# Kernel optimization log

Measured on AMD Instinct MI355X. Metric: run time of the kernel, lower is better.

Reference implementation:

```python
import jax, jax.numpy as jnp
import numpy as np

N_NODES = 100000
N_EDGES = 3200000
F_IN, F_HID, N_ACT = 128, 16, 32


def setup_inputs() -> dict:
    key = jax.random.key(0)
    k1, k2, k3, k4, k5, k6 = jax.random.split(key, 6)
    return {
        "x": jax.random.normal(k1, (N_NODES, F_IN), dtype=jnp.float32),
        "W1": jax.random.normal(k2, (F_IN, F_HID), dtype=jnp.float32) * 0.1,
        "b1": jax.random.normal(k3, (F_HID,), dtype=jnp.float32) * 0.1,
        "W2": jax.random.normal(k4, (F_HID, N_ACT), dtype=jnp.float32) * 0.1,
        "b2": jax.random.normal(k5, (N_ACT,), dtype=jnp.float32) * 0.1,
        "edge_index": jax.random.randint(k6, (2, N_EDGES), 0, N_NODES, dtype=jnp.int64),
    }


def _gcn_layer(h, W, b, src, dst, norm, n):
    # PyG GCNConv: linear first, then normalized scatter-add aggregation, then bias
    h = h @ W                                   # [N, out]
    msg = h[src] * norm[:, None]                # gather + edge scale, [E+N, out]
    agg = jax.ops.segment_sum(msg, dst, num_segments=n)
    return agg + b


def reference(x, W1, b1, W2, b2, edge_index):
    n = x.shape[0]
    loops = jnp.arange(n, dtype=edge_index.dtype)
    src = jnp.concatenate([edge_index[0], loops])  # add self-loops (GCNConv default)
    dst = jnp.concatenate([edge_index[1], loops])
    # symmetric normalization: deg on A + I, norm_e = d_src^-1/2 * d_dst^-1/2
    deg = jax.ops.segment_sum(jnp.ones_like(dst, dtype=x.dtype), dst, num_segments=n)
    dis = jnp.where(deg > 0, jax.lax.rsqrt(deg), 0.0)
    norm = dis[src] * dis[dst]
    h = jax.nn.relu(_gcn_layer(x, W1, b1, src, dst, norm, n))
    return _gcn_layer(h, W2, b2, src, dst, norm, n)
```

## Files before the change

### kernel.cpp

```cpp
#include <hip/hip_runtime.h>
#include <hip/hip_fp16.h>


#define NNODES 100000
#define FIN    128
#define FHID   16
#define NACT   32
#define BUCK   196
#define NB     511
#define MAGIC  21913099u
#define TILE   4096
#define ASTRIDE 17
#define SCALE    262144.0f
#define INVSCALE 3.814697265625e-06f

__device__ __forceinline__ int bucket_of(int d) {
    return (int)__umulhi((unsigned)d, MAGIC);
}

__device__ __forceinline__ unsigned pack2(float a, float b) {
    __half2 h = __floats2half2_rn(a, b);
    return *reinterpret_cast<unsigned*>(&h);
}

__device__ __forceinline__ float2 h2f(unsigned u) {
    return __half22float2(*reinterpret_cast<__half2*>(&u));
}

__device__ __forceinline__ int wave_iscan(int v, int lane) {
#pragma unroll
    for (int d = 1; d < 64; d <<= 1) {
        int u = __shfl_up(v, d, 64);
        if (lane >= d) v += u;
    }
    return v;
}

__global__ void k_coarse(const int* __restrict__ dst, int E, int* __restrict__ bcnt,
                         unsigned short* __restrict__ thist) {
    __shared__ int hist[NB];
    int t = threadIdx.x;
    int tb = blockIdx.x * TILE;
    int tn = min(TILE, E - tb);
    for (int i = t; i < NB; i += 256) hist[i] = 0;
    __syncthreads();
    if ((E & 3) == 0) {
        const int4* d4 = (const int4*)(dst + tb);
        int tn4 = tn >> 2;
        for (int i = t; i < tn4; i += 256) {
            int4 v = d4[i];
            atomicAdd(&hist[bucket_of(v.x)], 1);
            atomicAdd(&hist[bucket_of(v.y)], 1);
            atomicAdd(&hist[bucket_of(v.z)], 1);
            atomicAdd(&hist[bucket_of(v.w)], 1);
        }
        for (int i = (tn4 << 2) + t; i < tn; i += 256)
            atomicAdd(&hist[bucket_of(dst[tb + i])], 1);
    } else {
        for (int i = t; i < tn; i += 256)
            atomicAdd(&hist[bucket_of(dst[tb + i])], 1);
    }
    __syncthreads();
    size_t row = (size_t)blockIdx.x * NB;
    for (int i = t; i < NB; i += 256) {
        int hv = hist[i];
        thist[row + i] = (unsigned short)hv;
        if (hv) atomicAdd(&bcnt[i], hv);
    }
}

__global__ void __launch_bounds__(512) k_bin(
        const int* __restrict__ src, const int* __restrict__ dst, int E,
        const int* __restrict__ bcnt, int* __restrict__ gcur,
        const unsigned short* __restrict__ thist,
        int* __restrict__ bptr, unsigned* __restrict__ binned) {
    __shared__ unsigned staged[TILE];
    __shared__ int gscat[TILE];
    __shared__ int lcur[NB];
    __shared__ int dbase[NB];
    __shared__ int bptrS[NB];
    __shared__ int wsum[8];
    int t = threadIdx.x, lane = t & 63, wv = t >> 6;

    int c0 = (t < NB) ? bcnt[t] : 0;
    int incl0 = wave_iscan(c0, lane);
    if (lane == 63) wsum[wv] = incl0;
    __syncthreads();
    int add0 = 0;
#pragma unroll
    for (int i = 0; i < 8; ++i) add0 += (i < wv) ? wsum[i] : 0;
    incl0 += add0;
    int excl0 = incl0 - c0;
    if (t < NB) bptrS[t] = excl0;
    if (blockIdx.x == 0) {
        if (t < NB) bptr[t] = excl0;
        if (t == NB) bptr[NB] = excl0;
    }
    __syncthreads();

    int tb = blockIdx.x * TILE;
    int tn = min(TILE, E - tb);
    size_t row = (size_t)blockIdx.x * NB;
    int c = (t < NB) ? (int)thist[row + t] : 0;
    int incl = wave_iscan(c, lane);
    if (lane == 63) wsum[wv] = incl;
    __syncthreads();
    int add = 0;
#pragma unroll
    for (int i = 0; i < 8; ++i) add += (i < wv) ? wsum[i] : 0;
    incl += add;
    int excl = incl - c;
    if (t < NB) {
        lcur[t] = excl;
        int gb = (c > 0) ? atomicAdd(&gcur[t], c) : 0;
        dbase[t] = bptrS[t] + gb - excl;
    }
    __syncthreads();

    if ((E & 3) == 0) {
        const int4* d4 = (const int4*)(dst + tb);
        const int4* s4 = (const int4*)(src + tb);
        int tn4 = tn >> 2;
        for (int i = t; i < tn4; i += 512) {
            int4 dv = d4[i], sv = s4[i];
#pragma unroll
            for (int j = 0; j < 4; ++j) {
                int d = (j == 0) ? dv.x : (j == 1) ? dv.y : (j == 2) ? dv.z : dv.w;
                int s = (j == 0) ? sv.x : (j == 1) ? sv.y : (j == 2) ? sv.z : sv.w;
                int b = bucket_of(d);
                int pos = atomicAdd(&lcur[b], 1);
                staged[pos] = ((unsigned)s << 8) | (unsigned)(d - b * BUCK);
                gscat[pos] = dbase[b] + pos;
            }
        }
        for (int i = (tn4 << 2) + t; i < tn; i += 512) {
            int d = dst[tb + i], s = src[tb + i];
            int b = bucket_of(d);
            int pos = atomicAdd(&lcur[b], 1);
            staged[pos] = ((unsigned)s << 8) | (unsigned)(d - b * BUCK);
            gscat[pos] = dbase[b] + pos;
        }
    } else {
        for (int i = t; i < tn; i += 512) {
            int d = dst[tb + i], s = src[tb + i];
            int b = bucket_of(d);
            int pos = atomicAdd(&lcur[b], 1);
            staged[pos] = ((unsigned)s << 8) | (unsigned)(d - b * BUCK);
            gscat[pos] = dbase[b] + pos;
        }
    }
    __syncthreads();
    for (int j = t; j < tn; j += 512) binned[gscat[j]] = staged[j];
}

#define FMA4(A, S, W) { (A).x += (S) * (W).x; (A).y += (S) * (W).y; \
                        (A).z += (S) * (W).z; (A).w += (S) * (W).w; }

__global__ void __launch_bounds__(256) k_deg_xw1(
        const int* __restrict__ bptr, const unsigned* __restrict__ binned,
        const float* __restrict__ x, const float* __restrict__ W1,
        float* __restrict__ dis, __half* __restrict__ featp, int n) {
    __shared__ int cnt[BUCK];
    __shared__ float sdis[BUCK];
    int t = threadIdx.x;
    int bk = blockIdx.x;
    if (t < BUCK) cnt[t] = 0;
    __syncthreads();
    int beg = bptr[bk], end = bptr[bk + 1];
    for (int i = beg + t; i < end; i += 256) atomicAdd(&cnt[binned[i] & 255], 1);
    __syncthreads();
    int node = bk * BUCK + t;
    if (t < BUCK) {
        float dv = rsqrtf((float)cnt[t] + 1.0f);
        sdis[t] = dv;
        if (node < n) dis[node] = dv;
    }
    __syncthreads();
    if (t >= BUCK || node >= n) return;

    const float4* xr = (const float4*)(x + (size_t)node * FIN);
    const float4* w4 = (const float4*)W1;
    float4 a0 = make_float4(0.f, 0.f, 0.f, 0.f), a1 = a0, a2 = a0, a3 = a0;
#pragma unroll 8
    for (int k4 = 0; k4 < FIN / 4; ++k4) {
        float4 xv = xr[k4];
        int kb = k4 * 16;
        FMA4(a0, xv.x, w4[kb + 0]);  FMA4(a1, xv.x, w4[kb + 1]);
        FMA4(a2, xv.x, w4[kb + 2]);  FMA4(a3, xv.x, w4[kb + 3]);
        FMA4(a0, xv.y, w4[kb + 4]);  FMA4(a1, xv.y, w4[kb + 5]);
        FMA4(a2, xv.y, w4[kb + 6]);  FMA4(a3, xv.y, w4[kb + 7]);
        FMA4(a0, xv.z, w4[kb + 8]);  FMA4(a1, xv.z, w4[kb + 9]);
        FMA4(a2, xv.z, w4[kb + 10]); FMA4(a3, xv.z, w4[kb + 11]);
        FMA4(a0, xv.w, w4[kb + 12]); FMA4(a1, xv.w, w4[kb + 13]);
        FMA4(a2, xv.w, w4[kb + 14]); FMA4(a3, xv.w, w4[kb + 15]);
    }
    float d = sdis[t];
    uint4 w0, w1;
    w0.x = pack2(a0.x * d, a0.y * d); w0.y = pack2(a0.z * d, a0.w * d);
    w0.z = pack2(a1.x * d, a1.y * d); w0.w = pack2(a1.z * d, a1.w * d);
    w1.x = pack2(a2.x * d, a2.y * d); w1.y = pack2(a2.z * d, a2.w * d);
    w1.z = pack2(a3.x * d, a3.y * d); w1.w = pack2(a3.z * d, a3.w * d);
    uint4* hr = (uint4*)(featp + (size_t)node * FHID);
    hr[0] = w0; hr[1] = w1;
}

#define ADD8(U, dptr) { \
    float2 f0_ = h2f((U).x), f1_ = h2f((U).y), f2_ = h2f((U).z), f3_ = h2f((U).w); \
    atomicAdd(&(dptr)[0], __float2int_rn(f0_.x * SCALE)); \
    atomicAdd(&(dptr)[1], __float2int_rn(f0_.y * SCALE)); \
    atomicAdd(&(dptr)[2], __float2int_rn(f1_.x * SCALE)); \
    atomicAdd(&(dptr)[3], __float2int_rn(f1_.y * SCALE)); \
    atomicAdd(&(dptr)[4], __float2int_rn(f2_.x * SCALE)); \
    atomicAdd(&(dptr)[5], __float2int_rn(f2_.y * SCALE)); \
    atomicAdd(&(dptr)[6], __float2int_rn(f3_.x * SCALE)); \
    atomicAdd(&(dptr)[7], __float2int_rn(f3_.y * SCALE)); }

template <int L>
__global__ void __launch_bounds__(512) k_agg(
        const int* __restrict__ bptr, const unsigned* __restrict__ binned,
        const float* __restrict__ dis, const __half* __restrict__ featp,
        const float* __restrict__ W2, const float* __restrict__ bias,
        void* __restrict__ outp, int n) {
    __shared__ int acc[BUCK * ASTRIDE];
    __shared__ float wb[FHID * NACT];
    __shared__ float bs[NACT];
    int t = threadIdx.x;
    int bk = blockIdx.x;
    int base = bk * BUCK;
    int nn = min(BUCK, n - base);
    const uint4* fp4 = (const uint4*)featp;
    if (L == 2) {
        for (int i = t; i < FHID * NACT; i += 512) wb[i] = W2[i];
        if (t < NACT) bs[t] = bias[t];
    }
    for (int idx = t; idx < BUCK * 2; idx += 512) {
        int d = idx >> 1, p2 = idx & 1;
        int* a = &acc[d * ASTRIDE + p2 * 8];
        if (d < nn) {
            uint4 u = fp4[(size_t)((base + d) << 1) + p2];
            float2 f0 = h2f(u.x), f1 = h2f(u.y), f2 = h2f(u.z), f3 = h2f(u.w);
            a[0] = __float2int_rn(f0.x * SCALE);
            a[1] = __float2int_rn(f0.y * SCALE);
            a[2] = __float2int_rn(f1.x * SCALE);
            a[3] = __float2int_rn(f1.y * SCALE);
            a[4] = __float2int_rn(f2.x * SCALE);
            a[5] = __float2int_rn(f2.y * SCALE);
            a[6] = __float2int_rn(f3.x * SCALE);
            a[7] = __float2int_rn(f3.y * SCALE);
        } else {
            a[0] = 0; a[1] = 0; a[2] = 0; a[3] = 0;
            a[4] = 0; a[5] = 0; a[6] = 0; a[7] = 0;
        }
    }
    __syncthreads();
    int beg = bptr[bk], end = bptr[bk + 1];
    int pr = t >> 1, p2 = t & 1;
    int i = beg + pr;
    for (; i + 256 < end; i += 512) {
        unsigned e0 = binned[i];
        unsigned e1 = binned[i + 256];
        uint4 u0 = fp4[(size_t)((e0 >> 8) << 1) + p2];
        uint4 u1 = fp4[(size_t)((e1 >> 8) << 1) + p2];
        int* d0 = &acc[(int)(e0 & 255) * ASTRIDE + p2 * 8];
        ADD8(u0, d0);
        int* d1 = &acc[(int)(e1 & 255) * ASTRIDE + p2 * 8];
        ADD8(u1, d1);
    }
    if (i < end) {
        unsigned e0 = binned[i];
        uint4 u0 = fp4[(size_t)((e0 >> 8) << 1) + p2];
        int* d0 = &acc[(int)(e0 & 255) * ASTRIDE + p2 * 8];
        ADD8(u0, d0);
    }
    __syncthreads();
    if (L == 1) {
        for (int idx = t; idx < nn * 4; idx += 512) {
            int d = idx >> 2, pp = idx & 3;
            int node = base + d;
            float di = dis[node];
            const int* a = &acc[d * ASTRIDE + pp * 4];
            float4 bv = ((const float4*)bias)[pp];
            float f0 = (float)a[0] * INVSCALE;
            float f1 = (float)a[1] * INVSCALE;
            float f2 = (float)a[2] * INVSCALE;
            float f3 = (float)a[3] * INVSCALE;
            float rx = fmaxf(di * f0 + bv.x, 0.f) * di;
            float ry = fmaxf(di * f1 + bv.y, 0.f) * di;
            float rz = fmaxf(di * f2 + bv.z, 0.f) * di;
            float rw = fmaxf(di * f3 + bv.w, 0.f) * di;
            uint2 w;
            w.x = pack2(rx, ry);
            w.y = pack2(rz, rw);
            ((uint2*)outp)[(size_t)node * 4 + pp] = w;
        }
    } else {
        for (int idx = t; idx < nn * 2; idx += 512) {
            int d = idx >> 1, h = idx & 1;
            int node = base + d;
            float di = dis[node];
            float p16[FHID];
#pragma unroll
            for (int c = 0; c < FHID; ++c)
                p16[c] = di * ((float)acc[d * ASTRIDE + c] * INVSCALE);
            float o[16];
#pragma unroll
            for (int j = 0; j < 16; ++j) {
                int col = h * 16 + j;
                float s = bs[col];
#pragma unroll
                for (int c = 0; c < FHID; ++c) s += p16[c] * wb[c * NACT + col];
                o[j] = s;
            }
            float4* orow = (float4*)outp + (size_t)node * 8 + h * 4;
            orow[0] = make_float4(o[0], o[1], o[2], o[3]);
            orow[1] = make_float4(o[4], o[5], o[6], o[7]);
            orow[2] = make_float4(o[8], o[9], o[10], o[11]);
            orow[3] = make_float4(o[12], o[13], o[14], o[15]);
        }
    }
}

extern "C" void kernel_launch(void* const* d_in, const int* in_sizes, int n_in,
                              void* d_out, int out_size, void* d_ws, size_t ws_size,
                              hipStream_t stream) {
    const float* x  = (const float*)d_in[0];
    const float* W1 = (const float*)d_in[1];
    const float* b1 = (const float*)d_in[2];
    const float* W2 = (const float*)d_in[3];
    const float* b2 = (const float*)d_in[4];
    const int*   ei = (const int*)d_in[5];
    const int E = in_sizes[5] / 2;
    const int n = NNODES;
    const int npad = n + 8;
    const int* src = ei;
    const int* dst = ei + E;
    const int ntiles = (E + TILE - 1) / TILE;

    float* fb    = (float*)d_ws;
    float* dis   = fb;
    __half* featp = (__half*)(fb + (size_t)n);
    __half* h1p   = featp + (size_t)16 * npad;
    int*   ib    = (int*)(h1p + (size_t)16 * npad);
    int*   bcnt  = ib;
    int*   gcur  = ib + NB;
    int*   bptr  = ib + 2 * NB;
    size_t thist_off = (size_t)(3 * NB + 1);
    unsigned short* thist = (unsigned short*)(ib + thist_off);
    size_t thist_ints = ((size_t)ntiles * NB + 1) / 2;
    unsigned* binned = (unsigned*)(ib + thist_off + thist_ints);

    (void)hipMemsetAsync(bcnt, 0, 2 * NB * sizeof(int), stream);

    const int B = 256;
    k_coarse<<<ntiles, B, 0, stream>>>(dst, E, bcnt, thist);
    k_bin<<<ntiles, 512, 0, stream>>>(src, dst, E, bcnt, gcur, thist, bptr, binned);
    k_deg_xw1<<<NB, B, 0, stream>>>(bptr, binned, x, W1, dis, featp, n);
    k_agg<1><<<NB, 512, 0, stream>>>(bptr, binned, dis, featp, nullptr, b1, (void*)h1p, n);
    k_agg<2><<<NB, 512, 0, stream>>>(bptr, binned, dis, h1p, W2, b2, d_out, n);
}
```

Before: 214.9 us.

## Compute degrees via global atomics in coarse pass and double binning tile size

Per-node in-degrees are now counted with global atomics in the coarse histogram kernel, so the x@W1 kernel no longer rescans the binned edge list per bucket and can use a flat one-node-per-thread grid. The binning kernel now processes 8192-edge tiles with 1024 threads, merging two coarse tile histograms per block. This trades 3.2M scattered global atomics for removing a full pass over binned edges, and doubles shared memory per bin block, which may reduce occupancy.

```diff
diff --git a/kernel.cpp b/kernel.cpp
--- a/kernel.cpp
+++ b/kernel.cpp
@@ -10,6 +10,7 @@
 #define NB     511
 #define MAGIC  21913099u
 #define TILE   4096
+#define TILE2  8192
 #define ASTRIDE 17
 #define SCALE    262144.0f
 #define INVSCALE 3.814697265625e-06f
@@ -37,7 +38,7 @@
 }
 
 __global__ void k_coarse(const int* __restrict__ dst, int E, int* __restrict__ bcnt,
-                         unsigned short* __restrict__ thist) {
+                         int* __restrict__ deg, unsigned short* __restrict__ thist) {
     __shared__ int hist[NB];
     int t = threadIdx.x;
     int tb = blockIdx.x * TILE;
@@ -49,16 +50,20 @@
         int tn4 = tn >> 2;
         for (int i = t; i < tn4; i += 256) {
             int4 v = d4[i];
-            atomicAdd(&hist[bucket_of(v.x)], 1);
-            atomicAdd(&hist[bucket_of(v.y)], 1);
-            atomicAdd(&hist[bucket_of(v.z)], 1);
-            atomicAdd(&hist[bucket_of(v.w)], 1);
-        }
-        for (int i = (tn4 << 2) + t; i < tn; i += 256)
-            atomicAdd(&hist[bucket_of(dst[tb + i])], 1);
+            atomicAdd(&hist[bucket_of(v.x)], 1); atomicAdd(&deg[v.x], 1);
+            atomicAdd(&hist[bucket_of(v.y)], 1); atomicAdd(&deg[v.y], 1);
+            atomicAdd(&hist[bucket_of(v.z)], 1); atomicAdd(&deg[v.z], 1);
+            atomicAdd(&hist[bucket_of(v.w)], 1); atomicAdd(&deg[v.w], 1);
+        }
+        for (int i = (tn4 << 2) + t; i < tn; i += 256) {
+            int d = dst[tb + i];
+            atomicAdd(&hist[bucket_of(d)], 1); atomicAdd(&deg[d], 1);
+        }
     } else {
-        for (int i = t; i < tn; i += 256)
-            atomicAdd(&hist[bucket_of(dst[tb + i])], 1);
+        for (int i = t; i < tn; i += 256) {
+            int d = dst[tb + i];
+            atomicAdd(&hist[bucket_of(d)], 1); atomicAdd(&deg[d], 1);
+        }
     }
     __syncthreads();
     size_t row = (size_t)blockIdx.x * NB;
@@ -69,17 +74,17 @@
     }
 }
 
-__global__ void __launch_bounds__(512) k_bin(
+__global__ void __launch_bounds__(1024) k_bin(
         const int* __restrict__ src, const int* __restrict__ dst, int E,
         const int* __restrict__ bcnt, int* __restrict__ gcur,
         const unsigned short* __restrict__ thist,
         int* __restrict__ bptr, unsigned* __restrict__ binned) {
-    __shared__ unsigned staged[TILE];
-    __shared__ int gscat[TILE];
+    __shared__ unsigned staged[TILE2];
+    __shared__ int gscat[TILE2];
     __shared__ int lcur[NB];
     __shared__ int dbase[NB];
     __shared__ int bptrS[NB];
-    __shared__ int wsum[8];
+    __shared__ int wsum[16];
     int t = threadIdx.x, lane = t & 63, wv = t >> 6;
 
     int c0 = (t < NB) ? bcnt[t] : 0;
@@ -88,7 +93,7 @@
     __syncthreads();
     int add0 = 0;
 #pragma unroll
-    for (int i = 0; i < 8; ++i) add0 += (i < wv) ? wsum[i] : 0;
+    for (int i = 0; i < 16; ++i) add0 += (i < wv) ? wsum[i] : 0;
     incl0 += add0;
     int excl0 = incl0 - c0;
     if (t < NB) bptrS[t] = excl0;
@@ -98,16 +103,21 @@
     }
     __syncthreads();
 
-    int tb = blockIdx.x * TILE;
-    int tn = min(TILE, E - tb);
-    size_t row = (size_t)blockIdx.x * NB;
-    int c = (t < NB) ? (int)thist[row + t] : 0;
+    int ntc = (E + TILE - 1) / TILE;
+    int tb = blockIdx.x * TILE2;
+    int tn = min(TILE2, E - tb);
+    size_t row = (size_t)(2 * blockIdx.x) * NB;
+    int c = 0;
+    if (t < NB) {
+        c = (int)thist[row + t];
+        if (2 * blockIdx.x + 1 < ntc) c += (int)thist[row + NB + t];
+    }
     int incl = wave_iscan(c, lane);
     if (lane == 63) wsum[wv] = incl;
     __syncthreads();
     int add = 0;
 #pragma unroll
-    for (int i = 0; i < 8; ++i) add += (i < wv) ? wsum[i] : 0;
+    for (int i = 0; i < 16; ++i) add += (i < wv) ? wsum[i] : 0;
     incl += add;
     int excl = incl - c;
     if (t < NB) {
@@ -121,7 +131,7 @@
         const int4* d4 = (const int4*)(dst + tb);
         const int4* s4 = (const int4*)(src + tb);
         int tn4 = tn >> 2;
-        for (int i = t; i < tn4; i += 512) {
+        for (int i = t; i < tn4; i += 1024) {
             int4 dv = d4[i], sv = s4[i];
 #pragma unroll
             for (int j = 0; j < 4; ++j) {
@@ -133,7 +143,7 @@
                 gscat[pos] = dbase[b] + pos;
             }
         }
-        for (int i = (tn4 << 2) + t; i < tn; i += 512) {
+        for (int i = (tn4 << 2) + t; i < tn; i += 1024) {
             int d = dst[tb + i], s = src[tb + i];
             int b = bucket_of(d);
             int pos = atomicAdd(&lcur[b], 1);
@@ -141,7 +151,7 @@
             gscat[pos] = dbase[b] + pos;
         }
     } else {
-        for (int i = t; i < tn; i += 512) {
+        for (int i = t; i < tn; i += 1024) {
             int d = dst[tb + i], s = src[tb + i];
             int b = bucket_of(d);
             int pos = atomicAdd(&lcur[b], 1);
@@ -150,35 +160,21 @@
         }
     }
     __syncthreads();
-    for (int j = t; j < tn; j += 512) binned[gscat[j]] = staged[j];
+    for (int j = t; j < tn; j += 1024) binned[gscat[j]] = staged[j];
 }
 
 #define FMA4(A, S, W) { (A).x += (S) * (W).x; (A).y += (S) * (W).y; \
                         (A).z += (S) * (W).z; (A).w += (S) * (W).w; }
 
-__global__ void __launch_bounds__(256) k_deg_xw1(
-        const int* __restrict__ bptr, const unsigned* __restrict__ binned,
-        const float* __restrict__ x, const float* __restrict__ W1,
-        float* __restrict__ dis, __half* __restrict__ featp, int n) {
-    __shared__ int cnt[BUCK];
-    __shared__ float sdis[BUCK];
-    int t = threadIdx.x;
-    int bk = blockIdx.x;
-    if (t < BUCK) cnt[t] = 0;
-    __syncthreads();
-    int beg = bptr[bk], end = bptr[bk + 1];
-    for (int i = beg + t; i < end; i += 256) atomicAdd(&cnt[binned[i] & 255], 1);
-    __syncthreads();
-    int node = bk * BUCK + t;
-    if (t < BUCK) {
-        float dv = rsqrtf((float)cnt[t] + 1.0f);
-        sdis[t] = dv;
-        if (node < n) dis[node] = dv;
-    }
-    __syncthreads();
-    if (t >= BUCK || node >= n) return;
-
-    const float4* xr = (const float4*)(x + (size_t)node * FIN);
+__global__ void __launch_bounds__(256) k_xw1(
+        const int* __restrict__ deg, const float* __restrict__ x,
+        const float* __restrict__ W1, float* __restrict__ dis,
+        __half* __restrict__ featp, int n) {
+    int r = blockIdx.x * 256 + threadIdx.x;
+    if (r >= n) return;
+    float d = rsqrtf((float)deg[r] + 1.0f);
+    dis[r] = d;
+    const float4* xr = (const float4*)(x + (size_t)r * FIN);
     const float4* w4 = (const float4*)W1;
     float4 a0 = make_float4(0.f, 0.f, 0.f, 0.f), a1 = a0, a2 = a0, a3 = a0;
 #pragma unroll 8
@@ -194,13 +190,12 @@
         FMA4(a0, xv.w, w4[kb + 12]); FMA4(a1, xv.w, w4[kb + 13]);
         FMA4(a2, xv.w, w4[kb + 14]); FMA4(a3, xv.w, w4[kb + 15]);
     }
-    float d = sdis[t];
     uint4 w0, w1;
     w0.x = pack2(a0.x * d, a0.y * d); w0.y = pack2(a0.z * d, a0.w * d);
     w0.z = pack2(a1.x * d, a1.y * d); w0.w = pack2(a1.z * d, a1.w * d);
     w1.x = pack2(a2.x * d, a2.y * d); w1.y = pack2(a2.z * d, a2.w * d);
     w1.z = pack2(a3.x * d, a3.y * d); w1.w = pack2(a3.z * d, a3.w * d);
-    uint4* hr = (uint4*)(featp + (size_t)node * FHID);
+    uint4* hr = (uint4*)(featp + (size_t)r * FHID);
     hr[0] = w0; hr[1] = w1;
 }
 
@@ -334,7 +329,8 @@
     const int npad = n + 8;
     const int* src = ei;
     const int* dst = ei + E;
-    const int ntiles = (E + TILE - 1) / TILE;
+    const int ntc = (E + TILE - 1) / TILE;
+    const int ntb = (E + TILE2 - 1) / TILE2;
 
     float* fb    = (float*)d_ws;
     float* dis   = fb;
@@ -343,18 +339,19 @@
     int*   ib    = (int*)(h1p + (size_t)16 * npad);
     int*   bcnt  = ib;
     int*   gcur  = ib + NB;
-    int*   bptr  = ib + 2 * NB;
-    size_t thist_off = (size_t)(3 * NB + 1);
+    int*   deg   = ib + 2 * NB;
+    int*   bptr  = deg + n;
+    size_t thist_off = (size_t)(3 * NB + 1) + (size_t)n;
     unsigned short* thist = (unsigned short*)(ib + thist_off);
-    size_t thist_ints = ((size_t)ntiles * NB + 1) / 2;
+    size_t thist_ints = ((size_t)ntc * NB + 1) / 2;
     unsigned* binned = (unsigned*)(ib + thist_off + thist_ints);
 
-    (void)hipMemsetAsync(bcnt, 0, 2 * NB * sizeof(int), stream);
+    (void)hipMemsetAsync(bcnt, 0, (2 * NB + n) * sizeof(int), stream);
 
     const int B = 256;
-    k_coarse<<<ntiles, B, 0, stream>>>(dst, E, bcnt, thist);
-    k_bin<<<ntiles, 512, 0, stream>>>(src, dst, E, bcnt, gcur, thist, bptr, binned);
-    k_deg_xw1<<<NB, B, 0, stream>>>(bptr, binned, x, W1, dis, featp, n);
+    k_coarse<<<ntc, B, 0, stream>>>(dst, E, bcnt, deg, thist);
+    k_bin<<<ntb, 1024, 0, stream>>>(src, dst, E, bcnt, gcur, thist, bptr, binned);
+    k_xw1<<<(n + B - 1) / B, B, 0, stream>>>(deg, x, W1, dis, featp, n);
     k_agg<1><<<NB, 512, 0, stream>>>(bptr, binned, dis, featp, nullptr, b1, (void*)h1p, n);
     k_agg<2><<<NB, 512, 0, stream>>>(bptr, binned, dis, h1p, W2, b2, d_out, n);
 }
```

Result: slower. 323.1 us (+50.4%).
